# Performance work log

Measured on AMD Instinct MI355X. Metric: run time of the kernel, lower is better.

## Reference

```python
import jax, jax.numpy as jnp
import numpy as np

N_NODES = 100000
N_EDGES = 1600000
IN_CH = 64
HID = 64


def setup_inputs() -> dict:
    key = jax.random.key(0)
    ks = jax.random.split(key, 7)
    x = jax.random.normal(ks[0], (N_NODES, IN_CH), dtype=jnp.float32)
    edge_index = jax.random.randint(ks[1], (2, N_EDGES), 0, N_NODES, dtype=jnp.int64)
    node_pair = jax.random.randint(ks[2], (2,), 0, N_NODES, dtype=jnp.int64)
    W1 = jax.random.normal(ks[3], (IN_CH, HID), dtype=jnp.float32) / np.float32(np.sqrt(IN_CH))
    b1 = jnp.zeros((HID,), dtype=jnp.float32)
    W2 = jax.random.normal(ks[4], (HID, HID), dtype=jnp.float32) / np.float32(np.sqrt(HID))
    b2 = jnp.zeros((HID,), dtype=jnp.float32)
    fc_W = jax.random.normal(ks[5], (2 * HID, 1), dtype=jnp.float32) / np.float32(np.sqrt(2 * HID))
    fc_b = jnp.zeros((1,), dtype=jnp.float32)
    return {"x": x, "edge_index": edge_index, "node_pair": node_pair,
            "W1": W1, "b1": b1, "W2": W2, "b2": b2, "fc_W": fc_W, "fc_b": fc_b}


def gcn_conv(x, W, b, src, dst, n):
    # linear transform then symmetric-normalized scatter-add with self-loops (PyG GCNConv)
    h = x @ W                                   # [n, out]
    loop = jnp.arange(n, dtype=src.dtype)
    s = jnp.concatenate([src, loop])            # [E+n]
    d = jnp.concatenate([dst, loop])
    deg = jax.ops.segment_sum(jnp.ones_like(d, dtype=h.dtype), d, num_segments=n)
    dinv = jnp.where(deg > 0, jax.lax.rsqrt(deg), 0.0)
    norm = dinv[s] * dinv[d]                    # [E+n]
    out = jax.ops.segment_sum(h[s] * norm[:, None], d, num_segments=n)
    return out + b


def reference(x, edge_index, node_pair, W1, b1, W2, b2, fc_W, fc_b):
    src, dst = edge_index[0], edge_index[1]
    n = x.shape[0]
    h = jax.nn.relu(gcn_conv(x, W1, b1, src, dst, n))
    h = jax.nn.relu(gcn_conv(h, W2, b2, src, dst, n))
    z = jnp.concatenate([h[node_pair[0]], h[node_pair[1]]], axis=0)  # [2*HID]
    return jax.nn.sigmoid(z @ fc_W + fc_b)      # [1]
```

## Files before the change

kernel.cpp:

```cpp
#include <hip/hip_runtime.h>
#include <math.h>


#define CH 64
#define E1CAP 4096
#define F1CAP (E1CAP + 2)
#define E2CAP 131072
#define GRID 128
#define BLK 512
#define NWAVE (BLK / 64)
#define SPIN_MAX (1 << 20)

struct Params {
    const float* x;
    const int* src; const int* dst; const int* np_;
    const float* W1; const float* b1;
    const float* W2; const float* b2;
    const float* fcW; const float* fcb;
    int* bar;
    int* ctrl;
    int* deg;
    unsigned* bmF1; unsigned* bmNd;
    int* pos1; int* e1s; int* e1d; int* F1;
    int* e2s; int* e2d; float* h1; float* agg1e;
    float* out;
    int E; int N; int bmN;
};

__device__ __forceinline__ float dinv_of(int degv) {
    return rsqrtf((float)(degv + 1));
}

__device__ __forceinline__ void st_agent(int* p, int v) {
    __hip_atomic_store(p, v, __ATOMIC_RELAXED, __HIP_MEMORY_SCOPE_AGENT);
}
__device__ __forceinline__ void st_agent_f(float* p, float v) {
    __hip_atomic_store(p, v, __ATOMIC_RELAXED, __HIP_MEMORY_SCOPE_AGENT);
}
__device__ __forceinline__ int ld_agent(const int* p) {
    return __hip_atomic_load((int*)p, __ATOMIC_RELAXED, __HIP_MEMORY_SCOPE_AGENT);
}

__device__ __forceinline__ void gbar(int* bar, int phase) {
    __syncthreads();
    if (threadIdx.x == 0) {
        __builtin_amdgcn_fence(__ATOMIC_RELEASE, "agent");
        st_agent(&bar[blockIdx.x << 4], phase);
    }
    if (threadIdx.x < 64) {
        const int l = threadIdx.x;
        for (int it = 0; ; ++it) {
            int a = ld_agent(&bar[l << 4]);
            int b = ld_agent(&bar[(l + 64) << 4]);
            if (__all(a >= phase && b >= phase) || it > SPIN_MAX) break;
            __builtin_amdgcn_s_sleep(1);
        }
    }
    if (threadIdx.x == 0)
        __builtin_amdgcn_fence(__ATOMIC_ACQUIRE, "agent");
    __syncthreads();
}

__device__ __forceinline__ void reg_node(int u, unsigned* bmF1, unsigned* bmNd,
                                         int* ctrl, int* F1, int* pos1) {
    unsigned bit = 1u << (u & 31);
    unsigned old = atomicOr(&bmF1[u >> 5], bit);
    if (!(old & bit)) {
        atomicOr(&bmNd[u >> 5], bit);
        int i = atomicAdd(&ctrl[2], 1);
        st_agent(&F1[i], u);
        st_agent(&pos1[u], i);
    }
}

__device__ __forceinline__ void phase_e1f1(int gid, int gsz,
                                           const int* __restrict__ src,
                                           const int* __restrict__ dst, int E,
                                           int p0, int p1, int* ctrl,
                                           int* e1s, int* e1d,
                                           unsigned* bmF1, unsigned* bmNd,
                                           int* F1, int* pos1) {
    if (gid == 0) {
        reg_node(p0, bmF1, bmNd, ctrl, F1, pos1);
        if (p1 != p0) reg_node(p1, bmF1, bmNd, ctrl, F1, pos1);
    }
    const int nvec = E >> 2;
    const int4* dst4 = (const int4*)dst;
    for (int i = gid; i < nvec; i += gsz) {
        int4 d4 = dst4[i];
        int ds[4] = {d4.x, d4.y, d4.z, d4.w};
#pragma unroll
        for (int k = 0; k < 4; k++) {
            int d = ds[k];
            if (d == p0 || d == p1) {
                int s = src[i * 4 + k];
                int idx = atomicAdd(&ctrl[0], 1);
                if (idx < E1CAP) { st_agent(&e1s[idx], s); st_agent(&e1d[idx], d); }
                reg_node(s, bmF1, bmNd, ctrl, F1, pos1);
            }
        }
    }
    for (int e = (nvec << 2) + gid; e < E; e += gsz) {
        int d = dst[e];
        if (d == p0 || d == p1) {
            int s = src[e];
            int idx = atomicAdd(&ctrl[0], 1);
            if (idx < E1CAP) { st_agent(&e1s[idx], s); st_agent(&e1d[idx], d); }
            reg_node(s, bmF1, bmNd, ctrl, F1, pos1);
        }
    }
}

__device__ __forceinline__ void phase_e2(int gid, int gsz,
                                         const int* __restrict__ src,
                                         const int* __restrict__ dst, int E,
                                         const unsigned* __restrict__ bmF1,
                                         unsigned* bmNd, int* ctrl,
                                         int* e2s, int* e2d) {
    const int nvec = E >> 2;
    const int4* dst4 = (const int4*)dst;
    for (int i = gid; i < nvec; i += gsz) {
        int4 d4 = dst4[i];
        int ds[4] = {d4.x, d4.y, d4.z, d4.w};
#pragma unroll
        for (int k = 0; k < 4; k++) {
            int d = ds[k];
            if ((bmF1[d >> 5] >> (d & 31)) & 1u) {
                int s = src[i * 4 + k];
                atomicOr(&bmNd[s >> 5], 1u << (s & 31));
                int idx = atomicAdd(&ctrl[1], 1);
                if (idx < E2CAP) { st_agent(&e2s[idx], s); st_agent(&e2d[idx], d); }
            }
        }
    }
    for (int e = (nvec << 2) + gid; e < E; e += gsz) {
        int d = dst[e];
        if ((bmF1[d >> 5] >> (d & 31)) & 1u) {
            int s = src[e];
            atomicOr(&bmNd[s >> 5], 1u << (s & 31));
            int idx = atomicAdd(&ctrl[1], 1);
            if (idx < E2CAP) { st_agent(&e2s[idx], s); st_agent(&e2d[idx], d); }
        }
    }
}

__device__ __forceinline__ void phase_deg(int gid, int gsz,
                                          const int* __restrict__ dst, int E,
                                          const unsigned* __restrict__ bmNd,
                                          int* deg) {
    const int nvec = E >> 2;
    const int4* dst4 = (const int4*)dst;
    for (int i = gid; i < nvec; i += gsz) {
        int4 d4 = dst4[i];
        int ds[4] = {d4.x, d4.y, d4.z, d4.w};
#pragma unroll
        for (int k = 0; k < 4; k++) {
            int d = ds[k];
            if ((bmNd[d >> 5] >> (d & 31)) & 1u) atomicAdd(&deg[d], 1);
        }
    }
    for (int e = (nvec << 2) + gid; e < E; e += gsz) {
        int d = dst[e];
        if ((bmNd[d >> 5] >> (d & 31)) & 1u) atomicAdd(&deg[d], 1);
    }
}

__device__ __forceinline__ void phase_agg(int gid, int gsz,
                                          const float* __restrict__ x,
                                          const int* __restrict__ deg,
                                          const int* __restrict__ pos1,
                                          const int* __restrict__ ctrl,
                                          const int* __restrict__ e2s,
                                          const int* __restrict__ e2d,
                                          float* __restrict__ agg1e) {
    int cnt2 = min(ctrl[1], E2CAP);
    int total = cnt2 << 6;
    for (int idx = gid; idx < total; idx += gsz) {
        int e = idx >> 6, c = idx & 63;
        int s = e2s[e], u = e2d[e];
        float nrm = dinv_of(deg[s]) * dinv_of(deg[u]);
        atomicAdd(&agg1e[pos1[u] * CH + c], nrm * x[(size_t)s * CH + c]);
    }
}

__device__ __forceinline__ void phase_h1g(int blockId, int nBlocks, int tid,
                                          const float* __restrict__ x,
                                          const float* __restrict__ W1,
                                          const float* __restrict__ b1,
                                          const int* __restrict__ deg,
                                          const int* __restrict__ F1,
                                          const int* __restrict__ ctrl,
                                          const float* __restrict__ agg1e,
                                          float* __restrict__ h1,
                                          float (*a)[CH]) {
    int nf1 = min(ctrl[2], F1CAP);
    int w = tid >> 6, j = tid & 63;
    for (int i = blockId * NWAVE + w; i < nf1; i += nBlocks * NWAVE) {
        int u = F1[i];
        float du = dinv_of(deg[u]);
        a[w][j] = agg1e[i * CH + j] + du * du * x[(size_t)u * CH + j];
        float sum = b1[j];
#pragma unroll
        for (int k = 0; k < CH; k++) sum += a[w][k] * W1[k * CH + j];
        st_agent_f(&h1[i * CH + j], fmaxf(sum, 0.f));
    }
}

__device__ __forceinline__ void phase_tail(int tid,
                                           const float* __restrict__ h1,
                                           const int* __restrict__ deg,
                                           const int* __restrict__ pos1,
                                           const int* __restrict__ np_,
                                           const int* __restrict__ ctrl,
                                           const int* __restrict__ e1s,
                                           const int* __restrict__ e1d,
                                           const float* __restrict__ W2,
                                           const float* __restrict__ b2,
                                           const float* __restrict__ fcW,
                                           const float* __restrict__ fcb,
                                           float* __restrict__ out,
                                           float (*a2p)[CH], float (*a2)[CH],
                                           float* partial) {
    int w = tid >> 6, j = tid & 63;
    int t = w >> 2, sub = w & 3;
    int pp = np_[t];
    float dp = dinv_of(deg[pp]);
    float acc = (sub == 0) ? dp * dp * h1[pos1[pp] * CH + j] : 0.f;
    int cnt1 = min(ctrl[0], E1CAP);
    for (int e = sub; e < cnt1; e += 4) {
        if (e1d[e] == pp) {
            int s = e1s[e];
            acc += dinv_of(deg[s]) * dp * h1[pos1[s] * CH + j];
        }
    }
    a2p[w][j] = acc;
    __syncthreads();
    if (tid < 128) {
        int t2 = tid >> 6;
        a2[t2][j] = a2p[t2 * 4][j] + a2p[t2 * 4 + 1][j] +
                    a2p[t2 * 4 + 2][j] + a2p[t2 * 4 + 3][j];
    }
    __syncthreads();
    if (tid < 128) {
        int t2 = tid >> 6;
        float sum = b2[j];
#pragma unroll
        for (int k = 0; k < CH; k++) sum += a2[t2][k] * W2[k * CH + j];
        float v = fmaxf(sum, 0.f);
        float pr = v * fcW[t2 * CH + j];
        for (int off = 32; off > 0; off >>= 1) pr += __shfl_down(pr, off);
        if (j == 0) partial[t2] = pr;
    }
    __syncthreads();
    if (tid == 0) {
        float z = partial[0] + partial[1] + fcb[0];
        out[0] = 1.f / (1.f + expf(-z));
    }
}

__global__ __launch_bounds__(BLK, 1) void k_fused(Params p) {
    __shared__ float a[NWAVE][CH];
    __shared__ float a2p[NWAVE][CH];
    __shared__ float a2[2][CH];
    __shared__ float partial[2];
    const int gid = blockIdx.x * BLK + threadIdx.x;
    const int gsz = GRID * BLK;

    phase_e1f1(gid, gsz, p.src, p.dst, p.E, p.np_[0], p.np_[1], p.ctrl,
               p.e1s, p.e1d, p.bmF1, p.bmNd, p.F1, p.pos1);
    gbar(p.bar, 1);
    phase_e2(gid, gsz, p.src, p.dst, p.E, p.bmF1, p.bmNd, p.ctrl, p.e2s, p.e2d);
    gbar(p.bar, 2);
    phase_deg(gid, gsz, p.dst, p.E, p.bmNd, p.deg);
    gbar(p.bar, 3);
    phase_agg(gid, gsz, p.x, p.deg, p.pos1, p.ctrl, p.e2s, p.e2d, p.agg1e);
    gbar(p.bar, 4);
    phase_h1g(blockIdx.x, GRID, threadIdx.x, p.x, p.W1, p.b1, p.deg, p.F1,
              p.ctrl, p.agg1e, p.h1, a);
    gbar(p.bar, 5);
    if (blockIdx.x == 0)
        phase_tail(threadIdx.x, p.h1, p.deg, p.pos1, p.np_, p.ctrl, p.e1s, p.e1d,
                   p.W2, p.b2, p.fcW, p.fcb, p.out, a2p, a2, partial);
}

extern "C" void kernel_launch(void* const* d_in, const int* in_sizes, int n_in,
                              void* d_out, int out_size, void* d_ws, size_t ws_size,
                              hipStream_t stream) {
    const float* x   = (const float*)d_in[0];
    const int*   ei  = (const int*)d_in[1];
    const int*   np_ = (const int*)d_in[2];

    const int N = in_sizes[0] / CH;
    const int E = in_sizes[1] / 2;
    const int bmN = (N + 31) / 32;

    char* w = (char*)d_ws;
    size_t off = 0;
    auto alloc = [&](size_t bytes) {
        size_t o = off;
        off = (off + bytes + 255) & ~((size_t)255);
        return o;
    };
    size_t o_bar  = alloc((size_t)GRID * 16 * 4);
    size_t o_ctrl = alloc(64);
    size_t o_bmF1 = alloc((size_t)bmN * 4);
    size_t o_bmNd = alloc((size_t)bmN * 4);
    size_t o_deg  = alloc((size_t)N * 4);
    size_t o_agg  = alloc((size_t)F1CAP * CH * 4);
    size_t zero_end = off;
    size_t o_pos  = alloc((size_t)N * 4);
    size_t o_e1s  = alloc((size_t)E1CAP * 4);
    size_t o_e1d  = alloc((size_t)E1CAP * 4);
    size_t o_F1   = alloc((size_t)F1CAP * 4);
    size_t o_e2s  = alloc((size_t)E2CAP * 4);
    size_t o_e2d  = alloc((size_t)E2CAP * 4);
    size_t o_h1   = alloc((size_t)F1CAP * CH * 4);
    (void)ws_size;

    Params p;
    p.x    = x;
    p.src  = ei;
    p.dst  = ei + E;
    p.np_  = np_;
    p.W1   = (const float*)d_in[3];
    p.b1   = (const float*)d_in[4];
    p.W2   = (const float*)d_in[5];
    p.b2   = (const float*)d_in[6];
    p.fcW  = (const float*)d_in[7];
    p.fcb  = (const float*)d_in[8];
    p.bar   = (int*)(w + o_bar);
    p.ctrl  = (int*)(w + o_ctrl);
    p.bmF1  = (unsigned*)(w + o_bmF1);
    p.bmNd  = (unsigned*)(w + o_bmNd);
    p.deg   = (int*)(w + o_deg);
    p.agg1e = (float*)(w + o_agg);
    p.pos1  = (int*)(w + o_pos);
    p.e1s   = (int*)(w + o_e1s);
    p.e1d   = (int*)(w + o_e1d);
    p.F1    = (int*)(w + o_F1);
    p.e2s   = (int*)(w + o_e2s);
    p.e2d   = (int*)(w + o_e2d);
    p.h1    = (float*)(w + o_h1);
    p.out  = (float*)d_out;
    p.E = E; p.N = N; p.bmN = bmN;

    (void)hipMemsetAsync(d_ws, 0, zero_end, stream);

    k_fused<<<GRID, BLK, 0, stream>>>(p);
}
```

Baseline: 136.8 us.

## Run aggregation and tail in block 0 and drop two grid barriers

Once the degree phase finishes, the final aggregation, the first-layer transform and the tail now run inside block 0 only. That removes two grid-wide barriers, and the other blocks exit right after arriving at barrier 3. Zeroing of the degree array moves into the first phase and zeroing of the aggregation buffer moves into block 0, which shrinks the host memset. The grid doubles to 256 blocks and the barrier polls four slots per lane. The risks are serialising the small aggregation on one block and needing all 256 blocks co-resident for the spin barrier.

```diff
diff --git a/kernel.cpp b/kernel.cpp
--- a/kernel.cpp
+++ b/kernel.cpp
@@ -6,7 +6,7 @@
 #define E1CAP 4096
 #define F1CAP (E1CAP + 2)
 #define E2CAP 131072
-#define GRID 128
+#define GRID 256
 #define BLK 512
 #define NWAVE (BLK / 64)
 #define SPIN_MAX (1 << 20)
@@ -40,25 +40,39 @@
 __device__ __forceinline__ int ld_agent(const int* p) {
     return __hip_atomic_load((int*)p, __ATOMIC_RELAXED, __HIP_MEMORY_SCOPE_AGENT);
 }
-
-__device__ __forceinline__ void gbar(int* bar, int phase) {
+__device__ __forceinline__ float ld_agent_f(const float* p) {
+    return __hip_atomic_load((float*)p, __ATOMIC_RELAXED, __HIP_MEMORY_SCOPE_AGENT);
+}
+
+__device__ __forceinline__ void gbar_arrive(int* bar, int phase) {
     __syncthreads();
     if (threadIdx.x == 0) {
         __builtin_amdgcn_fence(__ATOMIC_RELEASE, "agent");
         st_agent(&bar[blockIdx.x << 4], phase);
     }
+}
+
+__device__ __forceinline__ void gbar_wait(int* bar, int phase) {
     if (threadIdx.x < 64) {
         const int l = threadIdx.x;
         for (int it = 0; ; ++it) {
             int a = ld_agent(&bar[l << 4]);
             int b = ld_agent(&bar[(l + 64) << 4]);
-            if (__all(a >= phase && b >= phase) || it > SPIN_MAX) break;
+            int c = ld_agent(&bar[(l + 128) << 4]);
+            int d = ld_agent(&bar[(l + 192) << 4]);
+            int m = min(min(a, b), min(c, d));
+            if (__all(m >= phase) || it > SPIN_MAX) break;
             __builtin_amdgcn_s_sleep(1);
         }
     }
     if (threadIdx.x == 0)
         __builtin_amdgcn_fence(__ATOMIC_ACQUIRE, "agent");
     __syncthreads();
+}
+
+__device__ __forceinline__ void gbar(int* bar, int phase) {
+    gbar_arrive(bar, phase);
+    gbar_wait(bar, phase);
 }
 
 __device__ __forceinline__ void reg_node(int u, unsigned* bmF1, unsigned* bmNd,
@@ -76,10 +90,12 @@
 __device__ __forceinline__ void phase_e1f1(int gid, int gsz,
                                            const int* __restrict__ src,
                                            const int* __restrict__ dst, int E,
+                                           int N, int* deg,
                                            int p0, int p1, int* ctrl,
                                            int* e1s, int* e1d,
                                            unsigned* bmF1, unsigned* bmNd,
                                            int* F1, int* pos1) {
+    for (int i = gid; i < N; i += gsz) st_agent(&deg[i], 0);
     if (gid == 0) {
         reg_node(p0, bmF1, bmNd, ctrl, F1, pos1);
         if (p1 != p0) reg_node(p1, bmF1, bmNd, ctrl, F1, pos1);
@@ -165,75 +181,68 @@
     }
 }
 
-__device__ __forceinline__ void phase_agg(int gid, int gsz,
-                                          const float* __restrict__ x,
-                                          const int* __restrict__ deg,
-                                          const int* __restrict__ pos1,
-                                          const int* __restrict__ ctrl,
-                                          const int* __restrict__ e2s,
-                                          const int* __restrict__ e2d,
-                                          float* __restrict__ agg1e) {
-    int cnt2 = min(ctrl[1], E2CAP);
-    int total = cnt2 << 6;
-    for (int idx = gid; idx < total; idx += gsz) {
-        int e = idx >> 6, c = idx & 63;
-        int s = e2s[e], u = e2d[e];
-        float nrm = dinv_of(deg[s]) * dinv_of(deg[u]);
-        atomicAdd(&agg1e[pos1[u] * CH + c], nrm * x[(size_t)s * CH + c]);
-    }
-}
-
-__device__ __forceinline__ void phase_h1g(int blockId, int nBlocks, int tid,
-                                          const float* __restrict__ x,
-                                          const float* __restrict__ W1,
-                                          const float* __restrict__ b1,
-                                          const int* __restrict__ deg,
-                                          const int* __restrict__ F1,
-                                          const int* __restrict__ ctrl,
-                                          const float* __restrict__ agg1e,
-                                          float* __restrict__ h1,
-                                          float (*a)[CH]) {
-    int nf1 = min(ctrl[2], F1CAP);
-    int w = tid >> 6, j = tid & 63;
-    for (int i = blockId * NWAVE + w; i < nf1; i += nBlocks * NWAVE) {
+__device__ __forceinline__ void block0_tail(int tid,
+                                            const float* __restrict__ x,
+                                            const float* __restrict__ W1,
+                                            const float* __restrict__ b1,
+                                            const float* __restrict__ W2,
+                                            const float* __restrict__ b2,
+                                            const float* __restrict__ fcW,
+                                            const float* __restrict__ fcb,
+                                            const int* __restrict__ np_,
+                                            const int* __restrict__ ctrl,
+                                            const int* __restrict__ deg,
+                                            const int* __restrict__ pos1,
+                                            const int* __restrict__ F1,
+                                            const int* __restrict__ e1s,
+                                            const int* __restrict__ e1d,
+                                            const int* __restrict__ e2s,
+                                            const int* __restrict__ e2d,
+                                            float* __restrict__ agg1e,
+                                            float* __restrict__ h1,
+                                            float* __restrict__ out,
+                                            float (*a)[CH], float (*a2p)[CH],
+                                            float (*a2)[CH], float* partial) {
+    const int nf1  = min(ctrl[2], F1CAP);
+    const int cnt2 = min(ctrl[1], E2CAP);
+    const int cnt1 = min(ctrl[0], E1CAP);
+    const int w = tid >> 6, j = tid & 63;
+
+    for (int i = tid; i < nf1 * CH; i += BLK) st_agent_f(&agg1e[i], 0.f);
+    __syncthreads();
+    {
+        int total = cnt2 << 6;
+        for (int idx = tid; idx < total; idx += BLK) {
+            int e = idx >> 6, c = idx & 63;
+            int s = e2s[e], u = e2d[e];
+            float nrm = dinv_of(deg[s]) * dinv_of(deg[u]);
+            atomicAdd(&agg1e[pos1[u] * CH + c], nrm * x[(size_t)s * CH + c]);
+        }
+    }
+    __syncthreads();
+    for (int i = w; i < nf1; i += NWAVE) {
         int u = F1[i];
         float du = dinv_of(deg[u]);
-        a[w][j] = agg1e[i * CH + j] + du * du * x[(size_t)u * CH + j];
+        a[w][j] = ld_agent_f(&agg1e[i * CH + j]) + du * du * x[(size_t)u * CH + j];
         float sum = b1[j];
 #pragma unroll
         for (int k = 0; k < CH; k++) sum += a[w][k] * W1[k * CH + j];
-        st_agent_f(&h1[i * CH + j], fmaxf(sum, 0.f));
-    }
-}
-
-__device__ __forceinline__ void phase_tail(int tid,
-                                           const float* __restrict__ h1,
-                                           const int* __restrict__ deg,
-                                           const int* __restrict__ pos1,
-                                           const int* __restrict__ np_,
-                                           const int* __restrict__ ctrl,
-                                           const int* __restrict__ e1s,
-                                           const int* __restrict__ e1d,
-                                           const float* __restrict__ W2,
-                                           const float* __restrict__ b2,
-                                           const float* __restrict__ fcW,
-                                           const float* __restrict__ fcb,
-                                           float* __restrict__ out,
-                                           float (*a2p)[CH], float (*a2)[CH],
-                                           float* partial) {
-    int w = tid >> 6, j = tid & 63;
-    int t = w >> 2, sub = w & 3;
-    int pp = np_[t];
-    float dp = dinv_of(deg[pp]);
-    float acc = (sub == 0) ? dp * dp * h1[pos1[pp] * CH + j] : 0.f;
-    int cnt1 = min(ctrl[0], E1CAP);
-    for (int e = sub; e < cnt1; e += 4) {
-        if (e1d[e] == pp) {
-            int s = e1s[e];
-            acc += dinv_of(deg[s]) * dp * h1[pos1[s] * CH + j];
-        }
-    }
-    a2p[w][j] = acc;
+        h1[i * CH + j] = fmaxf(sum, 0.f);
+    }
+    __syncthreads();
+    {
+        int t = w >> 2, sub = w & 3;
+        int pp = np_[t];
+        float dp = dinv_of(deg[pp]);
+        float acc = (sub == 0) ? dp * dp * h1[pos1[pp] * CH + j] : 0.f;
+        for (int e = sub; e < cnt1; e += 4) {
+            if (e1d[e] == pp) {
+                int s = e1s[e];
+                acc += dinv_of(deg[s]) * dp * h1[pos1[s] * CH + j];
+            }
+        }
+        a2p[w][j] = acc;
+    }
     __syncthreads();
     if (tid < 128) {
         int t2 = tid >> 6;
@@ -266,21 +275,20 @@
     const int gid = blockIdx.x * BLK + threadIdx.x;
     const int gsz = GRID * BLK;
 
-    phase_e1f1(gid, gsz, p.src, p.dst, p.E, p.np_[0], p.np_[1], p.ctrl,
-               p.e1s, p.e1d, p.bmF1, p.bmNd, p.F1, p.pos1);
+    phase_e1f1(gid, gsz, p.src, p.dst, p.E, p.N, p.deg,
+               p.np_[0], p.np_[1], p.ctrl, p.e1s, p.e1d,
+               p.bmF1, p.bmNd, p.F1, p.pos1);
     gbar(p.bar, 1);
     phase_e2(gid, gsz, p.src, p.dst, p.E, p.bmF1, p.bmNd, p.ctrl, p.e2s, p.e2d);
     gbar(p.bar, 2);
     phase_deg(gid, gsz, p.dst, p.E, p.bmNd, p.deg);
-    gbar(p.bar, 3);
-    phase_agg(gid, gsz, p.x, p.deg, p.pos1, p.ctrl, p.e2s, p.e2d, p.agg1e);
-    gbar(p.bar, 4);
-    phase_h1g(blockIdx.x, GRID, threadIdx.x, p.x, p.W1, p.b1, p.deg, p.F1,
-              p.ctrl, p.agg1e, p.h1, a);
-    gbar(p.bar, 5);
-    if (blockIdx.x == 0)
-        phase_tail(threadIdx.x, p.h1, p.deg, p.pos1, p.np_, p.ctrl, p.e1s, p.e1d,
-                   p.W2, p.b2, p.fcW, p.fcb, p.out, a2p, a2, partial);
+    gbar_arrive(p.bar, 3);
+    if (blockIdx.x != 0) return;
+    gbar_wait(p.bar, 3);
+    block0_tail(threadIdx.x, p.x, p.W1, p.b1, p.W2, p.b2, p.fcW, p.fcb,
+                p.np_, p.ctrl, p.deg, p.pos1, p.F1, p.e1s, p.e1d,
+                p.e2s, p.e2d, p.agg1e, p.h1, (float*)p.out,
+                a, a2p, a2, partial);
 }
 
 extern "C" void kernel_launch(void* const* d_in, const int* in_sizes, int n_in,
@@ -305,9 +313,8 @@
     size_t o_ctrl = alloc(64);
     size_t o_bmF1 = alloc((size_t)bmN * 4);
     size_t o_bmNd = alloc((size_t)bmN * 4);
+    size_t zero_end = off;
     size_t o_deg  = alloc((size_t)N * 4);
-    size_t o_agg  = alloc((size_t)F1CAP * CH * 4);
-    size_t zero_end = off;
     size_t o_pos  = alloc((size_t)N * 4);
     size_t o_e1s  = alloc((size_t)E1CAP * 4);
     size_t o_e1d  = alloc((size_t)E1CAP * 4);
@@ -315,6 +322,7 @@
     size_t o_e2s  = alloc((size_t)E2CAP * 4);
     size_t o_e2d  = alloc((size_t)E2CAP * 4);
     size_t o_h1   = alloc((size_t)F1CAP * CH * 4);
+    size_t o_agg  = alloc((size_t)F1CAP * CH * 4);
     (void)ws_size;
 
     Params p;
@@ -333,7 +341,6 @@
     p.bmF1  = (unsigned*)(w + o_bmF1);
     p.bmNd  = (unsigned*)(w + o_bmNd);
     p.deg   = (int*)(w + o_deg);
-    p.agg1e = (float*)(w + o_agg);
     p.pos1  = (int*)(w + o_pos);
     p.e1s   = (int*)(w + o_e1s);
     p.e1d   = (int*)(w + o_e1d);
@@ -341,6 +348,7 @@
     p.e2s   = (int*)(w + o_e2s);
     p.e2d   = (int*)(w + o_e2d);
     p.h1    = (float*)(w + o_h1);
+    p.agg1e = (float*)(w + o_agg);
     p.out  = (float*)d_out;
     p.E = E; p.N = N; p.bmN = bmN;
 
```

Result: slower. 182.3 us (+33.3%).

## Drop barrier fences, fold self-loop into agg, and shrink final phases to few blocks

Applied to the files above, without the earlier changes.

Replaces the release/acquire fences in the grid barrier with agent-scope relaxed atomic loads and stores on cross-phase data, so the fences no longer have to flush caches. Moves the self-loop term into the edge aggregation phase, which lets the h1 GEMV run on only 8 blocks. Blocks beyond that only signal arrival at the last barrier and exit, and only block 0 waits before the tail. This cuts barrier latency and idle spinning. The cost is more atomic-scope loads, plus a correctness risk if relaxed atomics without fences do not give enough ordering.

```diff
diff --git a/kernel.cpp b/kernel.cpp
--- a/kernel.cpp
+++ b/kernel.cpp
@@ -9,6 +9,7 @@
 #define GRID 128
 #define BLK 512
 #define NWAVE (BLK / 64)
+#define NP5 8
 #define SPIN_MAX (1 << 20)
 
 struct Params {
@@ -40,25 +41,35 @@
 __device__ __forceinline__ int ld_agent(const int* p) {
     return __hip_atomic_load((int*)p, __ATOMIC_RELAXED, __HIP_MEMORY_SCOPE_AGENT);
 }
-
-__device__ __forceinline__ void gbar(int* bar, int phase) {
+__device__ __forceinline__ unsigned ld_agent_u(const unsigned* p) {
+    return __hip_atomic_load((unsigned*)p, __ATOMIC_RELAXED, __HIP_MEMORY_SCOPE_AGENT);
+}
+__device__ __forceinline__ float ld_agent_f(const float* p) {
+    return __hip_atomic_load((float*)p, __ATOMIC_RELAXED, __HIP_MEMORY_SCOPE_AGENT);
+}
+
+__device__ __forceinline__ void gbar_arrive(int* bar, int phase) {
     __syncthreads();
     if (threadIdx.x == 0) {
-        __builtin_amdgcn_fence(__ATOMIC_RELEASE, "agent");
+        asm volatile("" ::: "memory");
         st_agent(&bar[blockIdx.x << 4], phase);
     }
+}
+__device__ __forceinline__ void gbar_wait(int* bar, int phase) {
     if (threadIdx.x < 64) {
         const int l = threadIdx.x;
         for (int it = 0; ; ++it) {
             int a = ld_agent(&bar[l << 4]);
             int b = ld_agent(&bar[(l + 64) << 4]);
-            if (__all(a >= phase && b >= phase) || it > SPIN_MAX) break;
+            if (__all(min(a, b) >= phase) || it > SPIN_MAX) break;
             __builtin_amdgcn_s_sleep(1);
         }
     }
-    if (threadIdx.x == 0)
-        __builtin_amdgcn_fence(__ATOMIC_ACQUIRE, "agent");
-    __syncthreads();
+    __syncthreads();
+}
+__device__ __forceinline__ void gbar(int* bar, int phase) {
+    gbar_arrive(bar, phase);
+    gbar_wait(bar, phase);
 }
 
 __device__ __forceinline__ void reg_node(int u, unsigned* bmF1, unsigned* bmNd,
@@ -125,7 +136,7 @@
 #pragma unroll
         for (int k = 0; k < 4; k++) {
             int d = ds[k];
-            if ((bmF1[d >> 5] >> (d & 31)) & 1u) {
+            if ((ld_agent_u(&bmF1[d >> 5]) >> (d & 31)) & 1u) {
                 int s = src[i * 4 + k];
                 atomicOr(&bmNd[s >> 5], 1u << (s & 31));
                 int idx = atomicAdd(&ctrl[1], 1);
@@ -135,7 +146,7 @@
     }
     for (int e = (nvec << 2) + gid; e < E; e += gsz) {
         int d = dst[e];
-        if ((bmF1[d >> 5] >> (d & 31)) & 1u) {
+        if ((ld_agent_u(&bmF1[d >> 5]) >> (d & 31)) & 1u) {
             int s = src[e];
             atomicOr(&bmNd[s >> 5], 1u << (s & 31));
             int idx = atomicAdd(&ctrl[1], 1);
@@ -156,12 +167,12 @@
 #pragma unroll
         for (int k = 0; k < 4; k++) {
             int d = ds[k];
-            if ((bmNd[d >> 5] >> (d & 31)) & 1u) atomicAdd(&deg[d], 1);
+            if ((ld_agent_u(&bmNd[d >> 5]) >> (d & 31)) & 1u) atomicAdd(&deg[d], 1);
         }
     }
     for (int e = (nvec << 2) + gid; e < E; e += gsz) {
         int d = dst[e];
-        if ((bmNd[d >> 5] >> (d & 31)) & 1u) atomicAdd(&deg[d], 1);
+        if ((ld_agent_u(&bmNd[d >> 5]) >> (d & 31)) & 1u) atomicAdd(&deg[d], 1);
     }
 }
 
@@ -172,33 +183,41 @@
                                           const int* __restrict__ ctrl,
                                           const int* __restrict__ e2s,
                                           const int* __restrict__ e2d,
+                                          const int* __restrict__ F1,
                                           float* __restrict__ agg1e) {
-    int cnt2 = min(ctrl[1], E2CAP);
-    int total = cnt2 << 6;
+    int cnt2 = min(ld_agent(&ctrl[1]), E2CAP);
+    int nf1  = min(ld_agent(&ctrl[2]), F1CAP);
+    int total = (cnt2 + nf1) << 6;
     for (int idx = gid; idx < total; idx += gsz) {
         int e = idx >> 6, c = idx & 63;
-        int s = e2s[e], u = e2d[e];
-        float nrm = dinv_of(deg[s]) * dinv_of(deg[u]);
-        atomicAdd(&agg1e[pos1[u] * CH + c], nrm * x[(size_t)s * CH + c]);
-    }
-}
-
-__device__ __forceinline__ void phase_h1g(int blockId, int nBlocks, int tid,
-                                          const float* __restrict__ x,
+        int row; float val;
+        if (e < cnt2) {
+            int s = ld_agent(&e2s[e]), u = ld_agent(&e2d[e]);
+            float nrm = dinv_of(ld_agent(&deg[s])) * dinv_of(ld_agent(&deg[u]));
+            row = ld_agent(&pos1[u]);
+            val = nrm * x[(size_t)s * CH + c];
+        } else {
+            int i = e - cnt2;
+            int u = ld_agent(&F1[i]);
+            float du = dinv_of(ld_agent(&deg[u]));
+            row = i;
+            val = du * du * x[(size_t)u * CH + c];
+        }
+        atomicAdd(&agg1e[row * CH + c], val);
+    }
+}
+
+__device__ __forceinline__ void phase_h1g(int blockId, int tid,
                                           const float* __restrict__ W1,
                                           const float* __restrict__ b1,
-                                          const int* __restrict__ deg,
-                                          const int* __restrict__ F1,
                                           const int* __restrict__ ctrl,
                                           const float* __restrict__ agg1e,
                                           float* __restrict__ h1,
                                           float (*a)[CH]) {
-    int nf1 = min(ctrl[2], F1CAP);
+    int nf1 = min(ld_agent(&ctrl[2]), F1CAP);
     int w = tid >> 6, j = tid & 63;
-    for (int i = blockId * NWAVE + w; i < nf1; i += nBlocks * NWAVE) {
-        int u = F1[i];
-        float du = dinv_of(deg[u]);
-        a[w][j] = agg1e[i * CH + j] + du * du * x[(size_t)u * CH + j];
+    for (int i = blockId * NWAVE + w; i < nf1; i += NP5 * NWAVE) {
+        a[w][j] = ld_agent_f(&agg1e[i * CH + j]);
         float sum = b1[j];
 #pragma unroll
         for (int k = 0; k < CH; k++) sum += a[w][k] * W1[k * CH + j];
@@ -224,13 +243,14 @@
     int w = tid >> 6, j = tid & 63;
     int t = w >> 2, sub = w & 3;
     int pp = np_[t];
-    float dp = dinv_of(deg[pp]);
-    float acc = (sub == 0) ? dp * dp * h1[pos1[pp] * CH + j] : 0.f;
-    int cnt1 = min(ctrl[0], E1CAP);
+    float dp = dinv_of(ld_agent(&deg[pp]));
+    float acc = (sub == 0) ? dp * dp * ld_agent_f(&h1[ld_agent(&pos1[pp]) * CH + j]) : 0.f;
+    int cnt1 = min(ld_agent(&ctrl[0]), E1CAP);
     for (int e = sub; e < cnt1; e += 4) {
-        if (e1d[e] == pp) {
-            int s = e1s[e];
-            acc += dinv_of(deg[s]) * dp * h1[pos1[s] * CH + j];
+        if (ld_agent(&e1d[e]) == pp) {
+            int s = ld_agent(&e1s[e]);
+            acc += dinv_of(ld_agent(&deg[s])) * dp *
+                   ld_agent_f(&h1[ld_agent(&pos1[s]) * CH + j]);
         }
     }
     a2p[w][j] = acc;
@@ -273,14 +293,18 @@
     gbar(p.bar, 2);
     phase_deg(gid, gsz, p.dst, p.E, p.bmNd, p.deg);
     gbar(p.bar, 3);
-    phase_agg(gid, gsz, p.x, p.deg, p.pos1, p.ctrl, p.e2s, p.e2d, p.agg1e);
+    phase_agg(gid, gsz, p.x, p.deg, p.pos1, p.ctrl, p.e2s, p.e2d, p.F1, p.agg1e);
+    if (blockIdx.x >= NP5) {
+        gbar_arrive(p.bar, 5);
+        return;
+    }
     gbar(p.bar, 4);
-    phase_h1g(blockIdx.x, GRID, threadIdx.x, p.x, p.W1, p.b1, p.deg, p.F1,
-              p.ctrl, p.agg1e, p.h1, a);
-    gbar(p.bar, 5);
-    if (blockIdx.x == 0)
-        phase_tail(threadIdx.x, p.h1, p.deg, p.pos1, p.np_, p.ctrl, p.e1s, p.e1d,
-                   p.W2, p.b2, p.fcW, p.fcb, p.out, a2p, a2, partial);
+    phase_h1g(blockIdx.x, threadIdx.x, p.W1, p.b1, p.ctrl, p.agg1e, p.h1, a);
+    gbar_arrive(p.bar, 5);
+    if (blockIdx.x != 0) return;
+    gbar_wait(p.bar, 5);
+    phase_tail(threadIdx.x, p.h1, p.deg, p.pos1, p.np_, p.ctrl, p.e1s, p.e1d,
+               p.W2, p.b2, p.fcW, p.fcb, (float*)p.out, a2p, a2, partial);
 }
 
 extern "C" void kernel_launch(void* const* d_in, const int* in_sizes, int n_in,
```

Result: faster. 132.7 us (-3.0%).
